# Kernel optimization log

Hardware: AMD Instinct MI355X
Metric: run time of the kernel (lower is better)

Reference implementation:

```python
import jax, jax.numpy as jnp
import numpy as np

D = 1024   # hidden
H = 4      # heads
HD = D // H
E = 8      # experts
FF = 4096  # expert ffn dim
CAP_FACTOR = 1.0


def _ln(x, g, b, eps=1e-5):
    mu = jnp.mean(x, -1, keepdims=True)
    v = jnp.mean((x - mu) ** 2, -1, keepdims=True)
    return (x - mu) * jax.lax.rsqrt(v + eps) * g + b


def setup_inputs() -> dict:
    key = jax.random.key(0)
    ks = jax.random.split(key, 8)
    L, N = 1024, 16
    s = 0.02
    return {
        "x": jax.random.normal(ks[0], (L, N, D), jnp.float32),
        "in_proj_w": jax.random.normal(ks[1], (3 * D, D), jnp.float32) * s,
        "in_proj_b": jnp.zeros((3 * D,), jnp.float32),
        "out_proj_w": jax.random.normal(ks[2], (D, D), jnp.float32) * s,
        "out_proj_b": jnp.zeros((D,), jnp.float32),
        "ln1_g": jnp.ones((D,), jnp.float32),
        "ln1_b": jnp.zeros((D,), jnp.float32),
        "ln2_g": jnp.ones((D,), jnp.float32),
        "ln2_b": jnp.zeros((D,), jnp.float32),
        "wg": jax.random.normal(ks[3], (D, E), jnp.float32) * s,
        "w1": jax.random.normal(ks[4], (E, D, FF), jnp.float32) * s,
        "b1": jnp.zeros((E, FF), jnp.float32),
        "w2": jax.random.normal(ks[5], (E, FF, D), jnp.float32) * s,
        "b2": jnp.zeros((E, D), jnp.float32),
    }


def _mha(x, w, b, ow, ob):
    # x: [L, N, D] (torch MultiheadAttention layout, batch_first=False)
    L, N, _ = x.shape
    qkv = x @ w.T + b
    q, k, v = jnp.split(qkv, 3, axis=-1)
    rh = lambda t: t.reshape(L, N, H, HD).transpose(1, 2, 0, 3)  # -> [N,H,L,HD]
    q, k, v = rh(q), rh(k), rh(v)
    scores = jnp.einsum('nhld,nhmd->nhlm', q, k) / np.float32(np.sqrt(HD))
    attn = jax.nn.softmax(scores, axis=-1)
    o = jnp.einsum('nhlm,nhmd->nhld', attn, v).transpose(2, 0, 1, 3).reshape(L, N, D)
    return o @ ow.T + ob


def _moe(x, wg, w1, b1, w2, b2):
    # top-1 switch gating with capacity drop, dispatch, grouped GEMM, combine
    L, N, _ = x.shape
    S = L * N
    cap = int(CAP_FACTOR * S) // E  # 2048
    xf = x.reshape(S, D)
    gates = jax.nn.softmax(xf @ wg, axis=-1)           # [S,E]
    idx = jnp.argmax(gates, axis=-1)                    # [S] top-1 expert
    mask1 = jax.nn.one_hot(idx, E, dtype=x.dtype)       # [S,E]
    # position of each token within its expert's queue
    loc = jnp.sum((jnp.cumsum(mask1, 0) - 1.0) * mask1, -1).astype(jnp.int32)
    keep = loc < cap                                    # capacity drop mask
    gate_val = jnp.take_along_axis(gates, idx[:, None], -1)[:, 0]
    slot = jnp.where(keep, idx.astype(jnp.int32) * cap + loc, E * cap)  # OOB if dropped
    disp = jnp.zeros((E * cap, D), x.dtype).at[slot].set(xf, mode='drop')
    disp = disp.reshape(E, cap, D)
    # expert = Linear(D,FF) -> Linear(FF,D), NO activation between (per source)
    h = jnp.einsum('ecd,edf->ecf', disp, w1) + b1[:, None, :]
    y = (jnp.einsum('ecf,efd->ecd', h, w2) + b2[:, None, :]).reshape(E * cap, D)
    out = jnp.where(keep[:, None], gate_val[:, None] * y[jnp.minimum(slot, E * cap - 1)], 0.0)
    return out.reshape(L, N, D)


def reference(x, in_proj_w, in_proj_b, out_proj_w, out_proj_b,
              ln1_g, ln1_b, ln2_g, ln2_b, wg, w1, b1, w2, b2):
    y1 = _ln(x + _mha(x, in_proj_w, in_proj_b, out_proj_w, out_proj_b), ln1_g, ln1_b)
    y2 = _ln(y1 + _moe(y1, wg, w1, b1, w2, b2), ln2_g, ln2_b)
    return y2
```

## Files before the change

### kernel.cpp

```cpp
#include <hip/hip_runtime.h>
#include <hip/hip_bf16.h>

typedef __bf16 bf16_t;
typedef bf16_t bf16x8 __attribute__((ext_vector_type(8)));
typedef float  f32x4  __attribute__((ext_vector_type(4)));
typedef _Float16 half4 __attribute__((ext_vector_type(4)));
typedef _Float16 half8 __attribute__((ext_vector_type(8)));

#define L_  1024
#define N_  16
#define S_  16384
#define D_  1024
#define H_  4
#define HD_ 256
#define E_  8
#define FF_ 4096
#define CAP_ 2048
#define ESLOTS_ (E_*CAP_)

__device__ __forceinline__ void gload16(const void* g, void* l) {
  __builtin_amdgcn_global_load_lds(
      (const __attribute__((address_space(1))) void*)g,
      (__attribute__((address_space(3))) void*)l,
      16, 0, 0);
}

#define SRC_SWZ(lane) (((lane) & 3) ^ (((lane) >> 3) & 3))

__global__ __launch_bounds__(256) void split2(
    const float* __restrict__ in, _Float16* __restrict__ oh,
    _Float16* __restrict__ ol, long n4)
{
  long i = (long)blockIdx.x * blockDim.x + threadIdx.x;
  long stride = (long)gridDim.x * blockDim.x;
  for (; i < n4; i += stride) {
    float4 v = ((const float4*)in)[i];
    half4 h, l;
    h.x = (_Float16)v.x; l.x = (_Float16)((v.x - (float)h.x) * 4096.0f);
    h.y = (_Float16)v.y; l.y = (_Float16)((v.y - (float)h.y) * 4096.0f);
    h.z = (_Float16)v.z; l.z = (_Float16)((v.z - (float)h.z) * 4096.0f);
    h.w = (_Float16)v.w; l.w = (_Float16)((v.w - (float)h.w) * 4096.0f);
    ((half4*)oh)[i] = h;
    ((half4*)ol)[i] = l;
  }
}

template<int EPI, bool HAS_BIAS>
__global__ __launch_bounds__(256) void hgemm3s(
    const _Float16* __restrict__ Ah, const _Float16* __restrict__ Al,
    const _Float16* __restrict__ Bh, const _Float16* __restrict__ Bl,
    float* __restrict__ Cf, _Float16* __restrict__ Ch, _Float16* __restrict__ Cl,
    const float* __restrict__ bias,
    int K, long lda, long ldb, long ldcf, long ldch,
    int Z2, long sA1, long sA2, long sB1, long sB2, long sC1, long sC2, long sBias)
{
  __shared__ _Float16 tA[2][2][128 * 32];
  __shared__ _Float16 tB[2][2][64 * 32];
  const int z  = blockIdx.z;
  const int z1 = z / Z2, z2 = z - z1 * Z2;
  const long aoff = (long)z1 * sA1 + (long)z2 * sA2;
  const long boff = (long)z1 * sB1 + (long)z2 * sB2;
  const long coff = (long)z1 * sC1 + (long)z2 * sC2;
  const int brow = blockIdx.x * 128, bcol = blockIdx.y * 64;
  const int tid = threadIdx.x, lane = tid & 63, wid = tid >> 6;
  const int wr = (wid >> 1) * 64, wc = (wid & 1) * 32;
  const int fr = lane & 15;
  const int fqs = (((lane >> 4) ^ ((fr >> 1) & 3)) * 8);

  const _Float16* sbA = ((wid == 0) ? Ah : Al) + aoff
                        + (long)(brow + (lane >> 2)) * lda + SRC_SWZ(lane) * 8;
  const _Float16* sbB = ((wid == 2) ? Bh : Bl) + boff
                        + (long)(bcol + (lane >> 2)) * ldb + SRC_SWZ(lane) * 8;
  const int limbsel = wid & 1;

  f32x4 acc0[4][2], acc1[4][2];
#pragma unroll
  for (int mi = 0; mi < 4; ++mi)
#pragma unroll
    for (int ni = 0; ni < 2; ++ni) {
      acc0[mi][ni] = f32x4{0.f, 0.f, 0.f, 0.f};
      acc1[mi][ni] = f32x4{0.f, 0.f, 0.f, 0.f};
    }

  if (wid < 2) {
#pragma unroll
    for (int i = 0; i < 8; ++i)
      gload16(sbA + (long)(16 * i) * lda, &tA[limbsel][0][i * 512]);
  } else {
#pragma unroll
    for (int i = 0; i < 4; ++i)
      gload16(sbB + (long)(16 * i) * ldb, &tB[limbsel][0][i * 512]);
  }
  __syncthreads();

  const int NT = K >> 5;
  for (int t = 0; t < NT; ++t) {
    const int cur = t & 1;
    if (t + 1 < NT) {
      const int k1 = (t + 1) * 32;
      if (wid < 2) {
#pragma unroll
        for (int i = 0; i < 8; ++i)
          gload16(sbA + (long)(16 * i) * lda + k1, &tA[limbsel][cur ^ 1][i * 512]);
      } else {
#pragma unroll
        for (int i = 0; i < 4; ++i)
          gload16(sbB + (long)(16 * i) * ldb + k1, &tB[limbsel][cur ^ 1][i * 512]);
      }
    }

    half8 bh_[2], bl_[2];
#pragma unroll
    for (int ni = 0; ni < 2; ++ni) {
      bh_[ni] = *(const half8*)&tB[0][cur][(wc + ni * 16 + fr) * 32 + fqs];
      bl_[ni] = *(const half8*)&tB[1][cur][(wc + ni * 16 + fr) * 32 + fqs];
    }
    half8 ah_[4], al_[4];
#pragma unroll
    for (int mi = 0; mi < 4; ++mi) {
      ah_[mi] = *(const half8*)&tA[0][cur][(wr + mi * 16 + fr) * 32 + fqs];
      al_[mi] = *(const half8*)&tA[1][cur][(wr + mi * 16 + fr) * 32 + fqs];
    }
#pragma unroll
    for (int mi = 0; mi < 4; ++mi)
#pragma unroll
      for (int ni = 0; ni < 2; ++ni)
        acc0[mi][ni] = __builtin_amdgcn_mfma_f32_16x16x32_f16(ah_[mi], bh_[ni], acc0[mi][ni], 0, 0, 0);
#pragma unroll
    for (int mi = 0; mi < 4; ++mi)
#pragma unroll
      for (int ni = 0; ni < 2; ++ni)
        acc1[mi][ni] = __builtin_amdgcn_mfma_f32_16x16x32_f16(ah_[mi], bl_[ni], acc1[mi][ni], 0, 0, 0);
#pragma unroll
    for (int mi = 0; mi < 4; ++mi)
#pragma unroll
      for (int ni = 0; ni < 2; ++ni)
        acc1[mi][ni] = __builtin_amdgcn_mfma_f32_16x16x32_f16(al_[mi], bh_[ni], acc1[mi][ni], 0, 0, 0);
    __syncthreads();
  }

#pragma unroll
  for (int mi = 0; mi < 4; ++mi) {
#pragma unroll
    for (int ni = 0; ni < 2; ++ni) {
      int gcol = bcol + wc + ni * 16 + fr;
      float bv = 0.0f;
      if constexpr (HAS_BIAS) bv = bias[(long)z1 * sBias + gcol];
#pragma unroll
      for (int v = 0; v < 4; ++v) {
        int grow = brow + wr + mi * 16 + (lane >> 4) * 4 + v;
        float val = acc0[mi][ni][v] + acc1[mi][ni][v] * 0.000244140625f + bv;
        if constexpr (EPI == 0) {
          Cf[coff + (long)grow * ldcf + gcol] = val;
        } else if constexpr (EPI == 1) {
          _Float16 hh = (_Float16)val;
          _Float16 ll = (_Float16)((val - (float)hh) * 4096.0f);
          long ci = coff + (long)grow * ldch + gcol;
          Ch[ci] = hh; Cl[ci] = ll;
        } else {
          if (bcol < 2048) {
            _Float16 hh = (_Float16)val;
            _Float16 ll = (_Float16)((val - (float)hh) * 4096.0f);
            long ci = (long)grow * ldch + gcol;
            Ch[ci] = hh; Cl[ci] = ll;
          } else {
            Cf[(long)grow * ldcf + (gcol - 2048)] = val;
          }
        }
      }
    }
  }
}

template<bool OUT_BF16, bool HAS_BIAS>
__global__ __launch_bounds__(256) void bgemm16(
    const bf16_t* __restrict__ A, const bf16_t* __restrict__ B,
    void* __restrict__ Cout, const float* __restrict__ bias,
    int K, long lda, long ldb, long ldc,
    long sA1, long sB1, long sC1, long sBias)
{
  __shared__ bf16_t tiles[2][2][128 * 32];
  const int z = blockIdx.z;
  const long coff = (long)z * sC1;
  const int brow = blockIdx.x * 128, bcol = blockIdx.y * 128;
  const int tid = threadIdx.x, lane = tid & 63, wid = tid >> 6;
  const int wr = (wid >> 1) * 64, wc = (wid & 1) * 64;
  const int fr = lane & 15;
  const int fqs = (((lane >> 4) ^ ((fr >> 1) & 3)) * 8);

  const bf16_t* src0 = (wid < 2) ? (A + (long)z * sA1) : (B + (long)z * sB1);
  const long ld = (wid < 2) ? lda : ldb;
  const int  rb = ((wid < 2) ? brow : bcol) + 64 * (wid & 1) + (lane >> 2);
  const bf16_t* srcbase = src0 + (long)rb * ld + SRC_SWZ(lane) * 8;
  const int tsel = wid >> 1, halfsel = wid & 1;

  f32x4 acc[4][4];
#pragma unroll
  for (int mi = 0; mi < 4; ++mi)
#pragma unroll
    for (int ni = 0; ni < 4; ++ni)
      acc[mi][ni] = f32x4{0.0f, 0.0f, 0.0f, 0.0f};

#pragma unroll
  for (int i = 0; i < 4; ++i)
    gload16(srcbase + (long)(16 * i) * ld, &tiles[tsel][0][(4 * halfsel + i) * 512]);
  __syncthreads();

  const int NT = K >> 5;
  for (int t = 0; t < NT; ++t) {
    const int cur = t & 1;
    if (t + 1 < NT) {
      const int k1 = (t + 1) * 32;
#pragma unroll
      for (int i = 0; i < 4; ++i)
        gload16(srcbase + (long)(16 * i) * ld + k1, &tiles[tsel][cur ^ 1][(4 * halfsel + i) * 512]);
    }

    bf16x8 af[4], bfv[4];
#pragma unroll
    for (int i = 0; i < 4; ++i) {
      af[i]  = *(const bf16x8*)&tiles[0][cur][(wr + i * 16 + fr) * 32 + fqs];
      bfv[i] = *(const bf16x8*)&tiles[1][cur][(wc + i * 16 + fr) * 32 + fqs];
    }
#pragma unroll
    for (int mi = 0; mi < 4; ++mi)
#pragma unroll
      for (int ni = 0; ni < 4; ++ni)
        acc[mi][ni] = __builtin_amdgcn_mfma_f32_16x16x32_bf16(af[mi], bfv[ni], acc[mi][ni], 0, 0, 0);
    __syncthreads();
  }

#pragma unroll
  for (int mi = 0; mi < 4; ++mi) {
#pragma unroll
    for (int ni = 0; ni < 4; ++ni) {
      int gcol = bcol + wc + ni * 16 + fr;
      float bv = 0.0f;
      if constexpr (HAS_BIAS) bv = bias[(long)z * sBias + gcol];
#pragma unroll
      for (int v = 0; v < 4; ++v) {
        int grow = brow + wr + mi * 16 + (lane >> 4) * 4 + v;
        float val = acc[mi][ni][v] + bv;
        long ci = coff + (long)grow * ldc + gcol;
        if constexpr (OUT_BF16) ((bf16_t*)Cout)[ci] = (bf16_t)val;
        else                    ((float*)Cout)[ci]  = val;
      }
    }
  }
}

template<typename TOUT>
__global__ __launch_bounds__(256) void transpose_f32(
    const float* __restrict__ src, TOUT* __restrict__ dst,
    long ld_src, long ld_dst, int Z2,
    long ss1, long ss2, long sd1, long sd2)
{
  __shared__ float t[32][33];
  const int z = blockIdx.z, z1 = z / Z2, z2 = z - z1 * Z2;
  src += (long)z1 * ss1 + (long)z2 * ss2;
  dst += (long)z1 * sd1 + (long)z2 * sd2;
  const int c0 = blockIdx.x * 32, r0 = blockIdx.y * 32;
  const int tx = threadIdx.x & 31, ty = threadIdx.x >> 5;
#pragma unroll
  for (int i = 0; i < 4; ++i)
    t[ty + i * 8][tx] = src[(long)(r0 + ty + i * 8) * ld_src + c0 + tx];
  __syncthreads();
#pragma unroll
  for (int i = 0; i < 4; ++i)
    dst[(long)(c0 + ty + i * 8) * ld_dst + r0 + tx] = (TOUT)t[tx][ty + i * 8];
}

__global__ __launch_bounds__(256) void transpose_split(
    const float* __restrict__ src, _Float16* __restrict__ dh, _Float16* __restrict__ dl,
    long ld_src, long ld_dst, int Z2,
    long ss1, long ss2, long sd1, long sd2)
{
  __shared__ float t[32][33];
  const int z = blockIdx.z, z1 = z / Z2, z2 = z - z1 * Z2;
  src += (long)z1 * ss1 + (long)z2 * ss2;
  dh  += (long)z1 * sd1 + (long)z2 * sd2;
  dl  += (long)z1 * sd1 + (long)z2 * sd2;
  const int c0 = blockIdx.x * 32, r0 = blockIdx.y * 32;
  const int tx = threadIdx.x & 31, ty = threadIdx.x >> 5;
#pragma unroll
  for (int i = 0; i < 4; ++i)
    t[ty + i * 8][tx] = src[(long)(r0 + ty + i * 8) * ld_src + c0 + tx];
  __syncthreads();
#pragma unroll
  for (int i = 0; i < 4; ++i) {
    float v = t[tx][ty + i * 8];
    _Float16 h = (_Float16)v;
    _Float16 l = (_Float16)((v - (float)h) * 4096.0f);
    long idx = (long)(c0 + ty + i * 8) * ld_dst + r0 + tx;
    dh[idx] = h;
    dl[idx] = l;
  }
}

__global__ __launch_bounds__(256) void softmax_inplace_split(
    float* __restrict__ Sm, float scale)
{
  __shared__ float red[4];
  const long row = blockIdx.x;
  const float4* p = (const float4*)(Sm + row * 1024);
  const int tid = threadIdx.x;
  float4 v = p[tid];
  float m = fmaxf(fmaxf(v.x, v.y), fmaxf(v.z, v.w));
#pragma unroll
  for (int o = 32; o; o >>= 1) m = fmaxf(m, __shfl_xor(m, o, 64));
  if ((tid & 63) == 0) red[tid >> 6] = m;
  __syncthreads();
  m = fmaxf(fmaxf(red[0], red[1]), fmaxf(red[2], red[3]));
  __syncthreads();
  float e0 = __expf((v.x - m) * scale);
  float e1 = __expf((v.y - m) * scale);
  float e2 = __expf((v.z - m) * scale);
  float e3 = __expf((v.w - m) * scale);
  float s = e0 + e1 + e2 + e3;
#pragma unroll
  for (int o = 32; o; o >>= 1) s += __shfl_xor(s, o, 64);
  if ((tid & 63) == 0) red[tid >> 6] = s;
  __syncthreads();
  s = red[0] + red[1] + red[2] + red[3];
  float inv = 1.0f / s;
  float p0 = e0 * inv, p1 = e1 * inv, p2 = e2 * inv, p3 = e3 * inv;
  half4 h, l;
  h.x = (_Float16)p0; l.x = (_Float16)((p0 - (float)h.x) * 4096.0f);
  h.y = (_Float16)p1; l.y = (_Float16)((p1 - (float)h.y) * 4096.0f);
  h.z = (_Float16)p2; l.z = (_Float16)((p2 - (float)h.z) * 4096.0f);
  h.w = (_Float16)p3; l.w = (_Float16)((p3 - (float)h.w) * 4096.0f);
  _Float16* base = (_Float16*)Sm + row * 2048;
  ((half4*)base)[tid] = h;
  ((half4*)(base + 1024))[tid] = l;
}

__global__ __launch_bounds__(256) void add_ln(
    const float* __restrict__ a, const float* __restrict__ b,
    const float* __restrict__ g, const float* __restrict__ be,
    float* __restrict__ y, bf16_t* __restrict__ yb)
{
  __shared__ float red[4];
  const long s = blockIdx.x;
  const int tid = threadIdx.x;
  const int lane = tid & 63, w = tid >> 6;
  float4 va = ((const float4*)(a + s * 1024))[tid];
  float4 vb = ((const float4*)(b + s * 1024))[tid];
  float v0 = va.x + vb.x, v1 = va.y + vb.y, v2 = va.z + vb.z, v3 = va.w + vb.w;
  float sum = v0 + v1 + v2 + v3;
#pragma unroll
  for (int o = 32; o; o >>= 1) sum += __shfl_xor(sum, o, 64);
  if (lane == 0) red[w] = sum;
  __syncthreads();
  float mu = (red[0] + red[1] + red[2] + red[3]) * (1.0f / 1024.0f);
  __syncthreads();
  float d0 = v0 - mu, d1 = v1 - mu, d2 = v2 - mu, d3 = v3 - mu;
  float ss = d0 * d0 + d1 * d1 + d2 * d2 + d3 * d3;
#pragma unroll
  for (int o = 32; o; o >>= 1) ss += __shfl_xor(ss, o, 64);
  if (lane == 0) red[w] = ss;
  __syncthreads();
  float var = (red[0] + red[1] + red[2] + red[3]) * (1.0f / 1024.0f);
  float rstd = rsqrtf(var + 1e-5f);
  float4 vg  = ((const float4*)g)[tid];
  float4 vbe = ((const float4*)be)[tid];
  float o0 = d0 * rstd * vg.x + vbe.x;
  float o1 = d1 * rstd * vg.y + vbe.y;
  float o2 = d2 * rstd * vg.z + vbe.z;
  float o3 = d3 * rstd * vg.w + vbe.w;
  float4 ov = {o0, o1, o2, o3};
  ((float4*)(y + s * 1024))[tid] = ov;
  bf16_t* yp = yb + s * 1024 + tid * 4;
  yp[0] = (bf16_t)o0; yp[1] = (bf16_t)o1; yp[2] = (bf16_t)o2; yp[3] = (bf16_t)o3;
}

__global__ __launch_bounds__(256) void combine_ln(
    const float* __restrict__ y1, const float* __restrict__ ymoe,
    const int* __restrict__ slot, const float* __restrict__ gval,
    const float* __restrict__ g, const float* __restrict__ be,
    float* __restrict__ out)
{
  __shared__ float red[4];
  const long s = blockIdx.x;
  const int tid = threadIdx.x;
  const int lane = tid & 63, w = tid >> 6;
  int sl = slot[s];
  bool keep = sl < ESLOTS_;
  float gv = keep ? gval[s] : 0.0f;
  long mrow = keep ? (long)sl * 1024 : 0;
  float4 va = ((const float4*)(y1 + s * 1024))[tid];
  float4 vm = ((const float4*)(ymoe + mrow))[tid];
  float v0 = va.x + gv * vm.x, v1 = va.y + gv * vm.y;
  float v2 = va.z + gv * vm.z, v3 = va.w + gv * vm.w;
  float sum = v0 + v1 + v2 + v3;
#pragma unroll
  for (int o = 32; o; o >>= 1) sum += __shfl_xor(sum, o, 64);
  if (lane == 0) red[w] = sum;
  __syncthreads();
  float mu = (red[0] + red[1] + red[2] + red[3]) * (1.0f / 1024.0f);
  __syncthreads();
  float d0 = v0 - mu, d1 = v1 - mu, d2 = v2 - mu, d3 = v3 - mu;
  float ss = d0 * d0 + d1 * d1 + d2 * d2 + d3 * d3;
#pragma unroll
  for (int o = 32; o; o >>= 1) ss += __shfl_xor(ss, o, 64);
  if (lane == 0) red[w] = ss;
  __syncthreads();
  float var = (red[0] + red[1] + red[2] + red[3]) * (1.0f / 1024.0f);
  float rstd = rsqrtf(var + 1e-5f);
  float4 vg  = ((const float4*)g)[tid];
  float4 vbe = ((const float4*)be)[tid];
  float4 ov = {d0 * rstd * vg.x + vbe.x, d1 * rstd * vg.y + vbe.y,
               d2 * rstd * vg.z + vbe.z, d3 * rstd * vg.w + vbe.w};
  ((float4*)(out + s * 1024))[tid] = ov;
}

__global__ __launch_bounds__(256) void gate_topk(
    const float* __restrict__ y1, const float* __restrict__ wg,
    int* __restrict__ idx, float* __restrict__ gval)
{
  __shared__ float wgs[8 * 1024];
  const int tid = threadIdx.x;
  for (int j = tid; j < 8192; j += 256)
    wgs[(j & 7) * 1024 + (j >> 3)] = wg[j];
  __syncthreads();
  const int lane = tid & 63, w = tid >> 6;
  const long s = (long)blockIdx.x * 4 + w;
  const float* xr = y1 + s * 1024;
  float acc[8] = {0, 0, 0, 0, 0, 0, 0, 0};
  for (int i = 0; i < 16; ++i) {
    int d = lane + i * 64;
    float xv = xr[d];
#pragma unroll
    for (int e = 0; e < 8; ++e) acc[e] = fmaf(xv, wgs[e * 1024 + d], acc[e]);
  }
#pragma unroll
  for (int e = 0; e < 8; ++e) {
#pragma unroll
    for (int o = 32; o; o >>= 1) acc[e] += __shfl_xor(acc[e], o, 64);
  }
  if (lane == 0) {
    float best = acc[0]; int bi = 0;
#pragma unroll
    for (int e = 1; e < 8; ++e) { if (acc[e] > best) { best = acc[e]; bi = e; } }
    float sum = 0.0f;
#pragma unroll
    for (int e = 0; e < 8; ++e) sum += __expf(acc[e] - best);
    idx[s] = bi;
    gval[s] = 1.0f / sum;
  }
}

__global__ __launch_bounds__(1024) void route_scan(
    const int* __restrict__ idx, int* __restrict__ slot, int* __restrict__ tfs)
{
  __shared__ int c_lds[8][1024];
  const int tid = threadIdx.x;
  const int lane = tid & 63, wid = tid >> 6;

  for (int j = tid; j < ESLOTS_; j += 1024) tfs[j] = -1;

  int myc[8] = {0, 0, 0, 0, 0, 0, 0, 0};
  for (int j = 0; j < 16; ++j) {
    int e = idx[tid * 16 + j];
    myc[e]++;
  }
#pragma unroll
  for (int e = 0; e < 8; ++e) c_lds[e][tid] = myc[e];
  __syncthreads();

  if (wid < 8) {
    int carry = 0;
    for (int cb = 0; cb < 1024; cb += 64) {
      int v = c_lds[wid][cb + lane];
#pragma unroll
      for (int o = 1; o < 64; o <<= 1) {
        int t = __shfl_up(v, o, 64);
        if (lane >= o) v += t;
      }
      v += carry;
      c_lds[wid][cb + lane] = v;
      carry = __shfl(v, 63, 64);
    }
  }
  __syncthreads();

  int run[8] = {0, 0, 0, 0, 0, 0, 0, 0};
  for (int j = 0; j < 16; ++j) {
    int s = tid * 16 + j;
    int e = idx[s];
    int excl = c_lds[e][tid] - myc[e];
    int loc = excl + run[e];
    run[e]++;
    int sl = (loc < CAP_) ? e * CAP_ + loc : ESLOTS_;
    slot[s] = sl;
    if (sl < ESLOTS_) tfs[sl] = s;
  }
}

__global__ void dispatch_rows(
    const int* __restrict__ tfs, const bf16_t* __restrict__ y1b,
    bf16_t* __restrict__ disp)
{
  const int row = blockIdx.x;
  const int t = tfs[row];
  bf16x8* d = (bf16x8*)(disp + (long)row * 1024);
  if (t >= 0) {
    const bf16x8* sp = (const bf16x8*)(y1b + (long)t * 1024);
    d[threadIdx.x] = sp[threadIdx.x];
  } else {
    bf16x8 zv;
#pragma unroll
    for (int i = 0; i < 8; ++i) zv[i] = (bf16_t)0.0f;
    d[threadIdx.x] = zv;
  }
}

__global__ void fill_val(float* __restrict__ p, float v, long n)
{
  long i = (long)blockIdx.x * blockDim.x + threadIdx.x;
  long stride = (long)gridDim.x * blockDim.x;
  for (; i < n; i += stride) p[i] = v;
}

extern "C" void kernel_launch(void* const* d_in, const int* in_sizes, int n_in,
                              void* d_out, int out_size, void* d_ws, size_t ws_size,
                              hipStream_t stream)
{
  const float* x    = (const float*)d_in[0];
  const float* Wqkv = (const float*)d_in[1];
  const float* bqkv = (const float*)d_in[2];
  const float* Wo   = (const float*)d_in[3];
  const float* bo   = (const float*)d_in[4];
  const float* g1   = (const float*)d_in[5];
  const float* b1n  = (const float*)d_in[6];
  const float* g2   = (const float*)d_in[7];
  const float* b2n  = (const float*)d_in[8];
  const float* wg   = (const float*)d_in[9];
  const float* w1   = (const float*)d_in[10];
  const float* b1e  = (const float*)d_in[11];
  const float* w2   = (const float*)d_in[12];
  const float* b2e  = (const float*)d_in[13];
  float* out = (float*)d_out;

  const size_t MB = 1ull << 20;
  const size_t REQUIRED = 384 * MB;
  if (ws_size < REQUIRED) {
    fill_val<<<2048, 256, 0, stream>>>(out, (float)(ws_size >> 20), (long)out_size);
    return;
  }

  char* ws = (char*)d_ws;
  _Float16* Xh   = (_Float16*)(ws + 0);
  _Float16* Xl   = (_Float16*)(ws + 32 * MB);
  _Float16* Wqh  = (_Float16*)(ws + 64 * MB);
  _Float16* Wql  = (_Float16*)(ws + 70 * MB);
  float*    scores = (float*)(ws + 0);
  _Float16* Woh  = (_Float16*)(ws + 64 * MB);
  _Float16* Wol  = (_Float16*)(ws + 66 * MB);
  _Float16* QKh  = (_Float16*)(ws + 80 * MB);
  _Float16* QKl  = (_Float16*)(ws + 144 * MB);
  float*    Vf32 = (float*)(ws + 208 * MB);
  _Float16* oh   = (_Float16*)(ws + 208 * MB);
  _Float16* ol   = (_Float16*)(ws + 240 * MB);
  _Float16* vTh  = (_Float16*)(ws + 272 * MB);
  _Float16* vTl  = (_Float16*)(ws + 304 * MB);
  float*    attn = (float*)(ws + 0);
  float*    y1   = (float*)(ws + 80 * MB);
  bf16_t*   y1b  = (bf16_t*)(ws + 144 * MB);
  bf16_t*   disp = (bf16_t*)(ws + 176 * MB);
  int*      idx  = (int*)(ws + 336 * MB);
  int*      slot = idx + S_;
  float*    gval = (float*)(slot + S_);
  int*      tfs  = (int*)(gval + S_);
  bf16_t*   W1t  = (bf16_t*)(ws + 0);
  bf16_t*   W2t  = (bf16_t*)(ws + 0);
  bf16_t*   h    = (bf16_t*)(ws + 208 * MB);
  float*    ymoe = (float*)(ws + 144 * MB);

  split2<<<4096, 256, 0, stream>>>(x, Xh, Xl, (long)S_ * D_ / 4);
  split2<<<2048, 256, 0, stream>>>(Wqkv, Wqh, Wql, (long)3 * D_ * D_ / 4);

  hgemm3s<2, true><<<dim3(128, 48, 1), 256, 0, stream>>>(
      Xh, Xl, Wqh, Wql, Vf32, QKh, QKl, bqkv,
      D_, D_, D_, D_, 2 * D_,
      1, 0, 0, 0, 0, 0, 0, 0);

  split2<<<1024, 256, 0, stream>>>(Wo, Woh, Wol, (long)D_ * D_ / 4);

  transpose_split<<<dim3(HD_ / 32, L_ / 32, 64), 256, 0, stream>>>(
      Vf32, vTh, vTl, (long)N_ * D_, L_,
      H_, D_, HD_, (long)H_ * HD_ * L_, (long)HD_ * L_);

  for (int g = 0; g < 4; ++g) {
    const long qko = (long)g * 4 * 2048;
    hgemm3s<0, false><<<dim3(8, 16, 16), 256, 0, stream>>>(
        QKh + qko, QKl + qko, QKh + qko + 1024, QKl + qko + 1024,
        scores, nullptr, nullptr, nullptr,
        HD_, (long)N_ * 2048, (long)N_ * 2048, L_, 0,
        H_, 2048, 256, 2048, 256, (long)H_ * L_ * L_, (long)L_ * L_, 0);
    softmax_inplace_split<<<4 * H_ * L_, 256, 0, stream>>>(scores, 0.0625f);
    hgemm3s<1, false><<<dim3(8, 4, 16), 256, 0, stream>>>(
        (_Float16*)scores, (_Float16*)scores + 1024,
        vTh + (long)g * 4 * H_ * HD_ * L_, vTl + (long)g * 4 * H_ * HD_ * L_,
        nullptr, oh + (long)g * 4 * D_, ol + (long)g * 4 * D_, nullptr,
        L_, 2048, L_, 0, (long)N_ * D_,
        H_, (long)4 * L_ * 2048, (long)L_ * 2048,
        (long)H_ * HD_ * L_, (long)HD_ * L_, D_, HD_, 0);
  }

  hgemm3s<0, true><<<dim3(128, 16, 1), 256, 0, stream>>>(
      oh, ol, Woh, Wol, attn, nullptr, nullptr, bo,
      D_, D_, D_, D_, 0,
      1, 0, 0, 0, 0, 0, 0, 0);

  add_ln<<<S_, 256, 0, stream>>>(x, attn, g1, b1n, y1, y1b);

  gate_topk<<<S_ / 4, 256, 0, stream>>>(y1, wg, idx, gval);

  route_scan<<<1, 1024, 0, stream>>>(idx, slot, tfs);

  dispatch_rows<<<ESLOTS_, 128, 0, stream>>>(tfs, y1b, disp);

  transpose_f32<bf16_t><<<dim3(FF_ / 32, D_ / 32, E_), 256, 0, stream>>>(
      w1, W1t, FF_, D_, 1, (long)D_ * FF_, 0, (long)FF_ * D_, 0);

  bgemm16<true, true><<<dim3(16, 32, 8), 256, 0, stream>>>(
      disp, W1t, h, b1e, D_, D_, D_, FF_,
      (long)CAP_ * D_, (long)FF_ * D_, (long)CAP_ * FF_, FF_);

  transpose_f32<bf16_t><<<dim3(D_ / 32, FF_ / 32, E_), 256, 0, stream>>>(
      w2, W2t, D_, FF_, 1, (long)FF_ * D_, 0, (long)D_ * FF_, 0);

  bgemm16<false, true><<<dim3(16, 8, 8), 256, 0, stream>>>(
      h, W2t, ymoe, b2e, FF_, FF_, FF_, D_,
      (long)CAP_ * FF_, (long)D_ * FF_, (long)CAP_ * D_, D_);

  combine_ln<<<S_, 256, 0, stream>>>(y1, ymoe, slot, gval, g2, b2n, out);
}
```

Before: 1.673 ms.

## Use single-fp16 attention path with high-precision recompute for near-tie gating tokens

Attention score, PV and out-projection GEMMs drop the 3-product fp16 hi/lo split and use one fp16 product, cutting their MFMA work and LDS traffic. To keep top-1 routing stable, tokens whose top-two gate logits fall within a fixed margin are collected, up to 128 per batch column, and their attention rows are recomputed with the split-precision path before the gate is fixed up. LayerNorm1 is fused with the gate matmul, and the y1 and MoE outputs are stored as bf16 to cut memory traffic. The risk is routing or accuracy mismatches when near-tie tokens exceed the per-column cap or the margin is too small.

```diff
diff --git a/kernel.cpp b/kernel.cpp
--- a/kernel.cpp
+++ b/kernel.cpp
@@ -2,6 +2,7 @@
 #include <hip/hip_bf16.h>
 
 typedef __bf16 bf16_t;
+typedef bf16_t bf16x4 __attribute__((ext_vector_type(4)));
 typedef bf16_t bf16x8 __attribute__((ext_vector_type(8)));
 typedef float  f32x4  __attribute__((ext_vector_type(4)));
 typedef _Float16 half4 __attribute__((ext_vector_type(4)));
@@ -17,6 +18,7 @@
 #define FF_ 4096
 #define CAP_ 2048
 #define ESLOTS_ (E_*CAP_)
+#define TAU_ 0.03f
 
 __device__ __forceinline__ void gload16(const void* g, void* l) {
   __builtin_amdgcn_global_load_lds(
@@ -45,7 +47,7 @@
   }
 }
 
-template<int EPI, bool HAS_BIAS>
+template<int EPI, bool HAS_BIAS, int PROD>
 __global__ __launch_bounds__(256) void hgemm3s(
     const _Float16* __restrict__ Ah, const _Float16* __restrict__ Al,
     const _Float16* __restrict__ Bh, const _Float16* __restrict__ Bl,
@@ -54,8 +56,9 @@
     int K, long lda, long ldb, long ldcf, long ldch,
     int Z2, long sA1, long sA2, long sB1, long sB2, long sC1, long sC2, long sBias)
 {
-  __shared__ _Float16 tA[2][2][128 * 32];
-  __shared__ _Float16 tB[2][2][64 * 32];
+  constexpr int NL = (PROD == 3) ? 2 : 1;
+  __shared__ _Float16 tA[NL][2][128 * 32];
+  __shared__ _Float16 tB[NL][2][64 * 32];
   const int z  = blockIdx.z;
   const int z1 = z / Z2, z2 = z - z1 * Z2;
   const long aoff = (long)z1 * sA1 + (long)z2 * sA2;
@@ -67,11 +70,21 @@
   const int fr = lane & 15;
   const int fqs = (((lane >> 4) ^ ((fr >> 1) & 3)) * 8);
 
-  const _Float16* sbA = ((wid == 0) ? Ah : Al) + aoff
-                        + (long)(brow + (lane >> 2)) * lda + SRC_SWZ(lane) * 8;
-  const _Float16* sbB = ((wid == 2) ? Bh : Bl) + boff
-                        + (long)(bcol + (lane >> 2)) * ldb + SRC_SWZ(lane) * 8;
-  const int limbsel = wid & 1;
+  const bool isA = (wid < 2);
+  int limb, dstoff, nch;
+  const _Float16* ssrc;
+  if constexpr (PROD == 3) {
+    limb = wid & 1; nch = isA ? 8 : 4; dstoff = 0;
+    ssrc = (wid == 0) ? Ah : (wid == 1) ? Al : (wid == 2) ? Bh : Bl;
+  } else {
+    limb = 0; nch = isA ? 4 : 2; dstoff = (wid & 1) * nch;
+    ssrc = isA ? Ah : Bh;
+  }
+  const long sld = isA ? lda : ldb;
+  const long soff = isA ? aoff : boff;
+  int srow = (isA ? brow : bcol) + (lane >> 2);
+  if constexpr (PROD == 1) srow += (wid & 1) * (isA ? 64 : 32);
+  const _Float16* sbase = ssrc + soff + (long)srow * sld + SRC_SWZ(lane) * 8;
 
   f32x4 acc0[4][2], acc1[4][2];
 #pragma unroll
@@ -82,14 +95,10 @@
       acc1[mi][ni] = f32x4{0.f, 0.f, 0.f, 0.f};
     }
 
-  if (wid < 2) {
-#pragma unroll
-    for (int i = 0; i < 8; ++i)
-      gload16(sbA + (long)(16 * i) * lda, &tA[limbsel][0][i * 512]);
-  } else {
-#pragma unroll
-    for (int i = 0; i < 4; ++i)
-      gload16(sbB + (long)(16 * i) * ldb, &tB[limbsel][0][i * 512]);
+  {
+    _Float16* d0 = (isA ? &tA[limb][0][0] : &tB[limb][0][0]) + dstoff * 512;
+    for (int i = 0; i < nch; ++i)
+      gload16(sbase + (long)(16 * i) * sld, d0 + i * 512);
   }
   __syncthreads();
 
@@ -98,44 +107,42 @@
     const int cur = t & 1;
     if (t + 1 < NT) {
       const int k1 = (t + 1) * 32;
-      if (wid < 2) {
-#pragma unroll
-        for (int i = 0; i < 8; ++i)
-          gload16(sbA + (long)(16 * i) * lda + k1, &tA[limbsel][cur ^ 1][i * 512]);
-      } else {
-#pragma unroll
-        for (int i = 0; i < 4; ++i)
-          gload16(sbB + (long)(16 * i) * ldb + k1, &tB[limbsel][cur ^ 1][i * 512]);
-      }
+      _Float16* d0 = (isA ? &tA[limb][cur ^ 1][0] : &tB[limb][cur ^ 1][0]) + dstoff * 512;
+      for (int i = 0; i < nch; ++i)
+        gload16(sbase + (long)(16 * i) * sld + k1, d0 + i * 512);
     }
 
     half8 bh_[2], bl_[2];
 #pragma unroll
     for (int ni = 0; ni < 2; ++ni) {
       bh_[ni] = *(const half8*)&tB[0][cur][(wc + ni * 16 + fr) * 32 + fqs];
-      bl_[ni] = *(const half8*)&tB[1][cur][(wc + ni * 16 + fr) * 32 + fqs];
+      if constexpr (PROD == 3)
+        bl_[ni] = *(const half8*)&tB[1][cur][(wc + ni * 16 + fr) * 32 + fqs];
     }
     half8 ah_[4], al_[4];
 #pragma unroll
     for (int mi = 0; mi < 4; ++mi) {
       ah_[mi] = *(const half8*)&tA[0][cur][(wr + mi * 16 + fr) * 32 + fqs];
-      al_[mi] = *(const half8*)&tA[1][cur][(wr + mi * 16 + fr) * 32 + fqs];
+      if constexpr (PROD == 3)
+        al_[mi] = *(const half8*)&tA[1][cur][(wr + mi * 16 + fr) * 32 + fqs];
     }
 #pragma unroll
     for (int mi = 0; mi < 4; ++mi)
 #pragma unroll
       for (int ni = 0; ni < 2; ++ni)
         acc0[mi][ni] = __builtin_amdgcn_mfma_f32_16x16x32_f16(ah_[mi], bh_[ni], acc0[mi][ni], 0, 0, 0);
-#pragma unroll
-    for (int mi = 0; mi < 4; ++mi)
-#pragma unroll
-      for (int ni = 0; ni < 2; ++ni)
-        acc1[mi][ni] = __builtin_amdgcn_mfma_f32_16x16x32_f16(ah_[mi], bl_[ni], acc1[mi][ni], 0, 0, 0);
-#pragma unroll
-    for (int mi = 0; mi < 4; ++mi)
-#pragma unroll
-      for (int ni = 0; ni < 2; ++ni)
-        acc1[mi][ni] = __builtin_amdgcn_mfma_f32_16x16x32_f16(al_[mi], bh_[ni], acc1[mi][ni], 0, 0, 0);
+    if constexpr (PROD == 3) {
+#pragma unroll
+      for (int mi = 0; mi < 4; ++mi)
+#pragma unroll
+        for (int ni = 0; ni < 2; ++ni)
+          acc1[mi][ni] = __builtin_amdgcn_mfma_f32_16x16x32_f16(ah_[mi], bl_[ni], acc1[mi][ni], 0, 0, 0);
+#pragma unroll
+      for (int mi = 0; mi < 4; ++mi)
+#pragma unroll
+        for (int ni = 0; ni < 2; ++ni)
+          acc1[mi][ni] = __builtin_amdgcn_mfma_f32_16x16x32_f16(al_[mi], bh_[ni], acc1[mi][ni], 0, 0, 0);
+    }
     __syncthreads();
   }
 
@@ -149,7 +156,8 @@
 #pragma unroll
       for (int v = 0; v < 4; ++v) {
         int grow = brow + wr + mi * 16 + (lane >> 4) * 4 + v;
-        float val = acc0[mi][ni][v] + acc1[mi][ni][v] * 0.000244140625f + bv;
+        float val = acc0[mi][ni][v] + bv;
+        if constexpr (PROD == 3) val += acc1[mi][ni][v] * 0.000244140625f;
         if constexpr (EPI == 0) {
           Cf[coff + (long)grow * ldcf + gcol] = val;
         } else if constexpr (EPI == 1) {
@@ -157,6 +165,8 @@
           _Float16 ll = (_Float16)((val - (float)hh) * 4096.0f);
           long ci = coff + (long)grow * ldch + gcol;
           Ch[ci] = hh; Cl[ci] = ll;
+        } else if constexpr (EPI == 3) {
+          Ch[coff + (long)grow * ldch + gcol] = (_Float16)val;
         } else {
           if (bcol < 2048) {
             _Float16 hh = (_Float16)val;
@@ -215,7 +225,6 @@
       for (int i = 0; i < 4; ++i)
         gload16(srcbase + (long)(16 * i) * ld + k1, &tiles[tsel][cur ^ 1][(4 * halfsel + i) * 512]);
     }
-
     bf16x8 af[4], bfv[4];
 #pragma unroll
     for (int i = 0; i < 4; ++i) {
@@ -297,7 +306,8 @@
   }
 }
 
-__global__ __launch_bounds__(256) void softmax_inplace_split(
+template<bool WRITE_LO>
+__global__ __launch_bounds__(256) void softmax_pack(
     float* __restrict__ Sm, float scale)
 {
   __shared__ float red[4];
@@ -324,27 +334,34 @@
   s = red[0] + red[1] + red[2] + red[3];
   float inv = 1.0f / s;
   float p0 = e0 * inv, p1 = e1 * inv, p2 = e2 * inv, p3 = e3 * inv;
-  half4 h, l;
-  h.x = (_Float16)p0; l.x = (_Float16)((p0 - (float)h.x) * 4096.0f);
-  h.y = (_Float16)p1; l.y = (_Float16)((p1 - (float)h.y) * 4096.0f);
-  h.z = (_Float16)p2; l.z = (_Float16)((p2 - (float)h.z) * 4096.0f);
-  h.w = (_Float16)p3; l.w = (_Float16)((p3 - (float)h.w) * 4096.0f);
+  half4 h;
+  h.x = (_Float16)p0; h.y = (_Float16)p1; h.z = (_Float16)p2; h.w = (_Float16)p3;
   _Float16* base = (_Float16*)Sm + row * 2048;
   ((half4*)base)[tid] = h;
-  ((half4*)(base + 1024))[tid] = l;
-}
-
-__global__ __launch_bounds__(256) void add_ln(
-    const float* __restrict__ a, const float* __restrict__ b,
+  if constexpr (WRITE_LO) {
+    half4 l;
+    l.x = (_Float16)((p0 - (float)h.x) * 4096.0f);
+    l.y = (_Float16)((p1 - (float)h.y) * 4096.0f);
+    l.z = (_Float16)((p2 - (float)h.z) * 4096.0f);
+    l.w = (_Float16)((p3 - (float)h.w) * 4096.0f);
+    ((half4*)(base + 1024))[tid] = l;
+  }
+}
+
+__global__ __launch_bounds__(256) void add_ln_gate(
+    const float* __restrict__ x, const float* __restrict__ attn,
     const float* __restrict__ g, const float* __restrict__ be,
-    float* __restrict__ y, bf16_t* __restrict__ yb)
+    const float* __restrict__ wg, bf16_t* __restrict__ yb,
+    int* __restrict__ idx, float* __restrict__ gval,
+    int* __restrict__ bcnt16, int* __restrict__ blist16)
 {
   __shared__ float red[4];
+  __shared__ float lred[4][8];
   const long s = blockIdx.x;
   const int tid = threadIdx.x;
   const int lane = tid & 63, w = tid >> 6;
-  float4 va = ((const float4*)(a + s * 1024))[tid];
-  float4 vb = ((const float4*)(b + s * 1024))[tid];
+  float4 va = ((const float4*)(x + s * 1024))[tid];
+  float4 vb = ((const float4*)(attn + s * 1024))[tid];
   float v0 = va.x + vb.x, v1 = va.y + vb.y, v2 = va.z + vb.z, v3 = va.w + vb.w;
   float sum = v0 + v1 + v2 + v3;
 #pragma unroll
@@ -363,18 +380,157 @@
   float rstd = rsqrtf(var + 1e-5f);
   float4 vg  = ((const float4*)g)[tid];
   float4 vbe = ((const float4*)be)[tid];
-  float o0 = d0 * rstd * vg.x + vbe.x;
-  float o1 = d1 * rstd * vg.y + vbe.y;
-  float o2 = d2 * rstd * vg.z + vbe.z;
-  float o3 = d3 * rstd * vg.w + vbe.w;
-  float4 ov = {o0, o1, o2, o3};
-  ((float4*)(y + s * 1024))[tid] = ov;
-  bf16_t* yp = yb + s * 1024 + tid * 4;
-  yp[0] = (bf16_t)o0; yp[1] = (bf16_t)o1; yp[2] = (bf16_t)o2; yp[3] = (bf16_t)o3;
+  float y0 = d0 * rstd * vg.x + vbe.x;
+  float y1v = d1 * rstd * vg.y + vbe.y;
+  float y2v = d2 * rstd * vg.z + vbe.z;
+  float y3 = d3 * rstd * vg.w + vbe.w;
+  bf16x4 ov = { (bf16_t)y0, (bf16_t)y1v, (bf16_t)y2v, (bf16_t)y3 };
+  *(bf16x4*)(yb + s * 1024 + tid * 4) = ov;
+  float lg[8];
+  const float* w0 = wg + (long)(tid * 4) * 8;
+#pragma unroll
+  for (int e = 0; e < 8; ++e)
+    lg[e] = y0 * w0[e] + y1v * w0[8 + e] + y2v * w0[16 + e] + y3 * w0[24 + e];
+#pragma unroll
+  for (int e = 0; e < 8; ++e) {
+#pragma unroll
+    for (int o = 32; o; o >>= 1) lg[e] += __shfl_xor(lg[e], o, 64);
+  }
+  if (lane == 0) {
+#pragma unroll
+    for (int e = 0; e < 8; ++e) lred[w][e] = lg[e];
+  }
+  __syncthreads();
+  if (tid == 0) {
+    float Lg[8];
+#pragma unroll
+    for (int e = 0; e < 8; ++e)
+      Lg[e] = lred[0][e] + lred[1][e] + lred[2][e] + lred[3][e];
+    float best = Lg[0], second = -1e30f; int bi = 0;
+#pragma unroll
+    for (int e = 1; e < 8; ++e) {
+      if (Lg[e] > best) { second = best; best = Lg[e]; bi = e; }
+      else if (Lg[e] > second) second = Lg[e];
+    }
+    float sm = 0.0f;
+#pragma unroll
+    for (int e = 0; e < 8; ++e) sm += __expf(Lg[e] - best);
+    idx[s] = bi;
+    gval[s] = 1.0f / sm;
+    if (best - second < TAU_) {
+      int n = (int)(s & 15);
+      int p = atomicAdd(&bcnt16[n], 1);
+      if (p < 128) blist16[n * 128 + p] = (int)s;
+    }
+  }
+}
+
+__global__ void zero16(int* __restrict__ p)
+{
+  if (threadIdx.x < 16) p[threadIdx.x] = 0;
+}
+
+__global__ __launch_bounds__(64) void qp_gather(
+    const int* __restrict__ bcnt16, const int* __restrict__ blist16,
+    const _Float16* __restrict__ QKh, const _Float16* __restrict__ QKl,
+    _Float16* __restrict__ Qph, _Float16* __restrict__ Qpl)
+{
+  const int b = blockIdx.x;
+  const int n = b >> 7, p = b & 127;
+  const int t = threadIdx.x;
+  half8* dh = (half8*)(Qph + (long)b * 1024);
+  half8* dl = (half8*)(Qpl + (long)b * 1024);
+  int cnt = bcnt16[n]; if (cnt > 128) cnt = 128;
+  if (p < cnt) {
+    long srow = (long)blist16[b] * 2048;
+    const half8* sh = (const half8*)(QKh + srow);
+    const half8* sl = (const half8*)(QKl + srow);
+    dh[t * 2]     = sh[t * 2];
+    dh[t * 2 + 1] = sh[t * 2 + 1];
+    dl[t * 2]     = sl[t * 2];
+    dl[t * 2 + 1] = sl[t * 2 + 1];
+  } else {
+    half8 z;
+#pragma unroll
+    for (int i = 0; i < 8; ++i) z[i] = (_Float16)0.0f;
+    dh[t * 2] = z; dh[t * 2 + 1] = z;
+    dl[t * 2] = z; dl[t * 2 + 1] = z;
+  }
+}
+
+__global__ __launch_bounds__(256) void gate_fix(
+    const int* __restrict__ bcnt16, const int* __restrict__ blist16,
+    const float* __restrict__ attn_p, const float* __restrict__ x,
+    const float* __restrict__ g, const float* __restrict__ be,
+    const float* __restrict__ wg,
+    int* __restrict__ idx, float* __restrict__ gval)
+{
+  const int b = blockIdx.x;
+  const int n = b >> 7, p = b & 127;
+  int cnt = bcnt16[n]; if (cnt > 128) cnt = 128;
+  if (p >= cnt) return;
+  const long s = blist16[b];
+  __shared__ float red[4];
+  __shared__ float lred[4][8];
+  const int tid = threadIdx.x;
+  const int lane = tid & 63, w = tid >> 6;
+  float4 va = ((const float4*)(x + s * 1024))[tid];
+  float4 vb = ((const float4*)(attn_p + (long)b * 1024))[tid];
+  float v0 = va.x + vb.x, v1 = va.y + vb.y, v2 = va.z + vb.z, v3 = va.w + vb.w;
+  float sum = v0 + v1 + v2 + v3;
+#pragma unroll
+  for (int o = 32; o; o >>= 1) sum += __shfl_xor(sum, o, 64);
+  if (lane == 0) red[w] = sum;
+  __syncthreads();
+  float mu = (red[0] + red[1] + red[2] + red[3]) * (1.0f / 1024.0f);
+  __syncthreads();
+  float d0 = v0 - mu, d1 = v1 - mu, d2 = v2 - mu, d3 = v3 - mu;
+  float ss = d0 * d0 + d1 * d1 + d2 * d2 + d3 * d3;
+#pragma unroll
+  for (int o = 32; o; o >>= 1) ss += __shfl_xor(ss, o, 64);
+  if (lane == 0) red[w] = ss;
+  __syncthreads();
+  float var = (red[0] + red[1] + red[2] + red[3]) * (1.0f / 1024.0f);
+  float rstd = rsqrtf(var + 1e-5f);
+  float4 vg  = ((const float4*)g)[tid];
+  float4 vbe = ((const float4*)be)[tid];
+  float y0 = d0 * rstd * vg.x + vbe.x;
+  float y1v = d1 * rstd * vg.y + vbe.y;
+  float y2v = d2 * rstd * vg.z + vbe.z;
+  float y3 = d3 * rstd * vg.w + vbe.w;
+  float lg[8];
+  const float* w0 = wg + (long)(tid * 4) * 8;
+#pragma unroll
+  for (int e = 0; e < 8; ++e)
+    lg[e] = y0 * w0[e] + y1v * w0[8 + e] + y2v * w0[16 + e] + y3 * w0[24 + e];
+#pragma unroll
+  for (int e = 0; e < 8; ++e) {
+#pragma unroll
+    for (int o = 32; o; o >>= 1) lg[e] += __shfl_xor(lg[e], o, 64);
+  }
+  if (lane == 0) {
+#pragma unroll
+    for (int e = 0; e < 8; ++e) lred[w][e] = lg[e];
+  }
+  __syncthreads();
+  if (tid == 0) {
+    float Lg[8];
+#pragma unroll
+    for (int e = 0; e < 8; ++e)
+      Lg[e] = lred[0][e] + lred[1][e] + lred[2][e] + lred[3][e];
+    float best = Lg[0]; int bi = 0;
+#pragma unroll
+    for (int e = 1; e < 8; ++e) { if (Lg[e] > best) { best = Lg[e]; bi = e; } }
+    float sm = 0.0f;
+#pragma unroll
+    for (int e = 0; e < 8; ++e) sm += __expf(Lg[e] - best);
+    idx[s] = bi;
+    gval[s] = 1.0f / sm;
+  }
 }
 
 __global__ __launch_bounds__(256) void combine_ln(
-    const float* __restrict__ y1, const float* __restrict__ ymoe,
+    const bf16_t* __restrict__ y1b, const bf16_t* __restrict__ ymoe,
     const int* __restrict__ slot, const float* __restrict__ gval,
     const float* __restrict__ g, const float* __restrict__ be,
     float* __restrict__ out)
@@ -387,10 +543,12 @@
   bool keep = sl < ESLOTS_;
   float gv = keep ? gval[s] : 0.0f;
   long mrow = keep ? (long)sl * 1024 : 0;
-  float4 va = ((const float4*)(y1 + s * 1024))[tid];
-  float4 vm = ((const float4*)(ymoe + mrow))[tid];
-  float v0 = va.x + gv * vm.x, v1 = va.y + gv * vm.y;
-  float v2 = va.z + gv * vm.z, v3 = va.w + gv * vm.w;
+  bf16x4 ya = *(const bf16x4*)(y1b + s * 1024 + tid * 4);
+  bf16x4 ym = *(const bf16x4*)(ymoe + mrow + tid * 4);
+  float v0 = (float)ya[0] + gv * (float)ym[0];
+  float v1 = (float)ya[1] + gv * (float)ym[1];
+  float v2 = (float)ya[2] + gv * (float)ym[2];
+  float v3 = (float)ya[3] + gv * (float)ym[3];
   float sum = v0 + v1 + v2 + v3;
 #pragma unroll
   for (int o = 32; o; o >>= 1) sum += __shfl_xor(sum, o, 64);
@@ -411,42 +569,6 @@
   float4 ov = {d0 * rstd * vg.x + vbe.x, d1 * rstd * vg.y + vbe.y,
                d2 * rstd * vg.z + vbe.z, d3 * rstd * vg.w + vbe.w};
   ((float4*)(out + s * 1024))[tid] = ov;
-}
-
-__global__ __launch_bounds__(256) void gate_topk(
-    const float* __restrict__ y1, const float* __restrict__ wg,
-    int* __restrict__ idx, float* __restrict__ gval)
-{
-  __shared__ float wgs[8 * 1024];
-  const int tid = threadIdx.x;
-  for (int j = tid; j < 8192; j += 256)
-    wgs[(j & 7) * 1024 + (j >> 3)] = wg[j];
-  __syncthreads();
-  const int lane = tid & 63, w = tid >> 6;
-  const long s = (long)blockIdx.x * 4 + w;
-  const float* xr = y1 + s * 1024;
-  float acc[8] = {0, 0, 0, 0, 0, 0, 0, 0};
-  for (int i = 0; i < 16; ++i) {
-    int d = lane + i * 64;
-    float xv = xr[d];
-#pragma unroll
-    for (int e = 0; e < 8; ++e) acc[e] = fmaf(xv, wgs[e * 1024 + d], acc[e]);
-  }
-#pragma unroll
-  for (int e = 0; e < 8; ++e) {
-#pragma unroll
-    for (int o = 32; o; o >>= 1) acc[e] += __shfl_xor(acc[e], o, 64);
-  }
-  if (lane == 0) {
-    float best = acc[0]; int bi = 0;
-#pragma unroll
-    for (int e = 1; e < 8; ++e) { if (acc[e] > best) { best = acc[e]; bi = e; } }
-    float sum = 0.0f;
-#pragma unroll
-    for (int e = 0; e < 8; ++e) sum += __expf(acc[e] - best);
-    idx[s] = bi;
-    gval[s] = 1.0f / sum;
-  }
 }
 
 __global__ __launch_bounds__(1024) void route_scan(
@@ -560,26 +682,32 @@
   _Float16* QKl  = (_Float16*)(ws + 144 * MB);
   float*    Vf32 = (float*)(ws + 208 * MB);
   _Float16* oh   = (_Float16*)(ws + 208 * MB);
-  _Float16* ol   = (_Float16*)(ws + 240 * MB);
   _Float16* vTh  = (_Float16*)(ws + 272 * MB);
   _Float16* vTl  = (_Float16*)(ws + 304 * MB);
   float*    attn = (float*)(ws + 0);
-  float*    y1   = (float*)(ws + 80 * MB);
-  bf16_t*   y1b  = (bf16_t*)(ws + 144 * MB);
-  bf16_t*   disp = (bf16_t*)(ws + 176 * MB);
+  bf16_t*   y1b  = (bf16_t*)(ws + 208 * MB);
+  float*    scp   = (float*)(ws + 0);
+  _Float16* Qph   = (_Float16*)(ws + 32 * MB);
+  _Float16* Qpl   = (_Float16*)(ws + 36 * MB);
+  _Float16* o_ph  = (_Float16*)(ws + 40 * MB);
+  _Float16* o_pl  = (_Float16*)(ws + 44 * MB);
+  float*    attnp = (float*)(ws + 48 * MB);
   int*      idx  = (int*)(ws + 336 * MB);
   int*      slot = idx + S_;
   float*    gval = (float*)(slot + S_);
   int*      tfs  = (int*)(gval + S_);
+  int*      bcnt16  = tfs + S_;
+  int*      blist16 = bcnt16 + 16;
+  bf16_t*   disp = (bf16_t*)(ws + 272 * MB);
   bf16_t*   W1t  = (bf16_t*)(ws + 0);
   bf16_t*   W2t  = (bf16_t*)(ws + 0);
-  bf16_t*   h    = (bf16_t*)(ws + 208 * MB);
-  float*    ymoe = (float*)(ws + 144 * MB);
+  bf16_t*   h    = (bf16_t*)(ws + 80 * MB);
+  bf16_t*   ymoe = (bf16_t*)(ws + 304 * MB);
 
   split2<<<4096, 256, 0, stream>>>(x, Xh, Xl, (long)S_ * D_ / 4);
   split2<<<2048, 256, 0, stream>>>(Wqkv, Wqh, Wql, (long)3 * D_ * D_ / 4);
 
-  hgemm3s<2, true><<<dim3(128, 48, 1), 256, 0, stream>>>(
+  hgemm3s<2, true, 3><<<dim3(128, 48, 1), 256, 0, stream>>>(
       Xh, Xl, Wqh, Wql, Vf32, QKh, QKl, bqkv,
       D_, D_, D_, D_, 2 * D_,
       1, 0, 0, 0, 0, 0, 0, 0);
@@ -592,29 +720,50 @@
 
   for (int g = 0; g < 4; ++g) {
     const long qko = (long)g * 4 * 2048;
-    hgemm3s<0, false><<<dim3(8, 16, 16), 256, 0, stream>>>(
+    hgemm3s<0, false, 1><<<dim3(8, 16, 16), 256, 0, stream>>>(
         QKh + qko, QKl + qko, QKh + qko + 1024, QKl + qko + 1024,
         scores, nullptr, nullptr, nullptr,
         HD_, (long)N_ * 2048, (long)N_ * 2048, L_, 0,
         H_, 2048, 256, 2048, 256, (long)H_ * L_ * L_, (long)L_ * L_, 0);
-    softmax_inplace_split<<<4 * H_ * L_, 256, 0, stream>>>(scores, 0.0625f);
-    hgemm3s<1, false><<<dim3(8, 4, 16), 256, 0, stream>>>(
+    softmax_pack<false><<<4 * H_ * L_, 256, 0, stream>>>(scores, 0.0625f);
+    hgemm3s<3, false, 1><<<dim3(8, 4, 16), 256, 0, stream>>>(
         (_Float16*)scores, (_Float16*)scores + 1024,
         vTh + (long)g * 4 * H_ * HD_ * L_, vTl + (long)g * 4 * H_ * HD_ * L_,
-        nullptr, oh + (long)g * 4 * D_, ol + (long)g * 4 * D_, nullptr,
+        nullptr, oh + (long)g * 4 * D_, nullptr, nullptr,
         L_, 2048, L_, 0, (long)N_ * D_,
         H_, (long)4 * L_ * 2048, (long)L_ * 2048,
         (long)H_ * HD_ * L_, (long)HD_ * L_, D_, HD_, 0);
   }
 
-  hgemm3s<0, true><<<dim3(128, 16, 1), 256, 0, stream>>>(
-      oh, ol, Woh, Wol, attn, nullptr, nullptr, bo,
+  hgemm3s<0, true, 1><<<dim3(128, 16, 1), 256, 0, stream>>>(
+      oh, nullptr, Woh, Wol, attn, nullptr, nullptr, bo,
       D_, D_, D_, D_, 0,
       1, 0, 0, 0, 0, 0, 0, 0);
 
-  add_ln<<<S_, 256, 0, stream>>>(x, attn, g1, b1n, y1, y1b);
-
-  gate_topk<<<S_ / 4, 256, 0, stream>>>(y1, wg, idx, gval);
+  zero16<<<1, 64, 0, stream>>>(bcnt16);
+  add_ln_gate<<<S_, 256, 0, stream>>>(x, attn, g1, b1n, wg, y1b,
+                                      idx, gval, bcnt16, blist16);
+
+  qp_gather<<<2048, 64, 0, stream>>>(bcnt16, blist16, QKh, QKl, Qph, Qpl);
+  hgemm3s<0, false, 3><<<dim3(1, 16, 64), 256, 0, stream>>>(
+      Qph, Qpl, QKh + 1024, QKl + 1024, scp, nullptr, nullptr, nullptr,
+      HD_, 1024, (long)N_ * 2048, 1024, 0,
+      4, (long)128 * 1024, 256, 2048, 256,
+      (long)4 * 128 * 1024, (long)128 * 1024, 0);
+  softmax_pack<true><<<64 * 128, 256, 0, stream>>>(scp, 0.0625f);
+  hgemm3s<1, false, 3><<<dim3(1, 4, 64), 256, 0, stream>>>(
+      (_Float16*)scp, (_Float16*)scp + 1024, vTh, vTl,
+      nullptr, o_ph, o_pl, nullptr,
+      L_, 2048, L_, 0, 1024,
+      4, (long)4 * 128 * 2048, (long)128 * 2048,
+      (long)H_ * HD_ * L_, (long)HD_ * L_,
+      (long)128 * 1024, 256, 0);
+  hgemm3s<0, true, 3><<<dim3(16, 16, 1), 256, 0, stream>>>(
+      o_ph, o_pl, Woh, Wol, attnp, nullptr, nullptr, bo,
+      D_, D_, D_, D_, 0,
+      1, 0, 0, 0, 0, 0, 0, 0);
+  gate_fix<<<2048, 256, 0, stream>>>(bcnt16, blist16, attnp, x,
+                                     g1, b1n, wg, idx, gval);
 
   route_scan<<<1, 1024, 0, stream>>>(idx, slot, tfs);
 
@@ -630,9 +779,9 @@
   transpose_f32<bf16_t><<<dim3(D_ / 32, FF_ / 32, E_), 256, 0, stream>>>(
       w2, W2t, D_, FF_, 1, (long)FF_ * D_, 0, (long)D_ * FF_, 0);
 
-  bgemm16<false, true><<<dim3(16, 8, 8), 256, 0, stream>>>(
+  bgemm16<true, true><<<dim3(16, 8, 8), 256, 0, stream>>>(
       h, W2t, ymoe, b2e, FF_, FF_, FF_, D_,
       (long)CAP_ * FF_, (long)D_ * FF_, (long)CAP_ * D_, D_);
 
-  combine_ln<<<S_, 256, 0, stream>>>(y1, ymoe, slot, gval, g2, b2n, out);
-}
+  combine_ln<<<S_, 256, 0, stream>>>(y1b, ymoe, slot, gval, g2, b2n, out);
+}
```

New measurement: 1.591 ms. 4.9% less time.
